# Performance work log

Measured on AMD Instinct MI355X. Metric: run time of the kernel, lower is better.

The kernel has to match this reference:

```python
import jax, jax.numpy as jnp
import numpy as np

N_NODES = 50000
N_EDGES = 600000
IN_F, HID, OUT_F = 602, 128, 41


def _gconv(x, W, b, src, dst, n):
    # DGL GraphConv, norm='both': D_dst^{-1/2} A (D_src^{-1/2} x W) + b
    ones = jnp.ones(src.shape, dtype=x.dtype)
    deg_out = jnp.clip(jax.ops.segment_sum(ones, src, num_segments=n), 1.0)
    deg_in = jnp.clip(jax.ops.segment_sum(ones, dst, num_segments=n), 1.0)
    h = x * jax.lax.rsqrt(deg_out)[:, None]
    h = h @ W  # dense transform first (in_feats > out_feats path)
    agg = jax.ops.segment_sum(h[src], dst, num_segments=n)  # [N, out]
    return agg * jax.lax.rsqrt(deg_in)[:, None] + b


def setup_inputs() -> dict:
    key = jax.random.key(0)
    ks = jax.random.split(key, 8)
    features = jax.random.normal(ks[0], (N_NODES, IN_F), dtype=jnp.float32)
    src = jax.random.randint(ks[1], (N_EDGES,), 0, N_NODES, dtype=jnp.int32)
    dst = jax.random.randint(ks[2], (N_EDGES,), 0, N_NODES, dtype=jnp.int32)
    def glorot(k, fan_in, fan_out):
        s = jnp.sqrt(6.0 / (fan_in + fan_out)).astype(jnp.float32)
        return jax.random.uniform(k, (fan_in, fan_out), jnp.float32, -s, s)
    return {
        'features': features, 'src': src, 'dst': dst,
        'W1': glorot(ks[3], IN_F, HID), 'b1': jnp.zeros((HID,), jnp.float32),
        'W2': glorot(ks[4], HID, HID), 'b2': jnp.zeros((HID,), jnp.float32),
        'W3': glorot(ks[5], HID, HID), 'b3': jnp.zeros((HID,), jnp.float32),
        'Wfc': glorot(ks[6], HID, OUT_F), 'bfc': jnp.zeros((OUT_F,), jnp.float32),
    }


def reference(features, src, dst, W1, b1, W2, b2, W3, b3, Wfc, bfc):
    n = features.shape[0]
    relu = jax.nn.relu
    x = relu(_gconv(features, W1, b1, src, dst, n))  # x = _x
    _x = relu(_gconv(x, W2, b2, src, dst, n))        # branch (layer2)
    x = relu(_gconv(x, W2, b2, src, dst, n))         # main (same layer2)
    x = relu(_gconv(x, W3, b3, src, dst, n))         # layer3
    x = relu(x + _x)                                  # residual + relu
    return x @ Wfc + bfc
```

## Files before the change

### kernel.cpp

```cpp
#include <hip/hip_runtime.h>
#include <hip/hip_bf16.h>

#define NN   50000
#define NE   600000
#define INF  602
#define HID  128
#define OUTF 41
#define NBLK 196

#define GXCD   128
#define GBLKS  (8 * GXCD)
#define GCHUNKS (2 * GXCD)
#define GCHN   ((NN + GCHUNKS - 1) / GCHUNKS)

typedef __attribute__((ext_vector_type(8))) short bf16x8;
typedef __attribute__((ext_vector_type(4))) float f32x4;
typedef __attribute__((ext_vector_type(2))) int i32x2;

__device__ inline unsigned short f2bf(float x) {
    unsigned u = __float_as_uint(x);
    unsigned r = u + 0x7FFF + ((u >> 16) & 1);
    return (unsigned short)(r >> 16);
}

#define GLL16(gp, lp) \
    __builtin_amdgcn_global_load_lds((const __attribute__((address_space(1))) unsigned int*)(gp), \
                                     (__attribute__((address_space(3))) unsigned int*)(lp), 16, 0, 0)

__global__ __launch_bounds__(256) void deg_hist_k(const int* __restrict__ src,
                                                  const int* __restrict__ dst,
                                                  int* __restrict__ cnt_out,
                                                  int* __restrict__ cnt_in, int E) {
    int e = blockIdx.x * 256 + threadIdx.x;
    if (e < E) {
        atomicAdd(&cnt_out[src[e]], 1);
        atomicAdd(&cnt_in[dst[e]], 1);
    }
}

__global__ __launch_bounds__(256) void scan1_k(const int* __restrict__ cnt,
                                               int* __restrict__ rowptr,
                                               int* __restrict__ blockSum) {
    __shared__ int tmp[256];
    int tid = threadIdx.x;
    int i = blockIdx.x * 256 + tid;
    int v = (i < NN) ? cnt[i] : 0;
    tmp[tid] = v;
    __syncthreads();
#pragma unroll
    for (int off = 1; off < 256; off <<= 1) {
        int t = (tid >= off) ? tmp[tid - off] : 0;
        __syncthreads();
        tmp[tid] += t;
        __syncthreads();
    }
    if (i < NN) rowptr[i] = tmp[tid] - v;
    if (tid == 255) blockSum[blockIdx.x] = tmp[255];
}

__global__ __launch_bounds__(256) void scan23_k(int* __restrict__ rowptr,
                                                const int* __restrict__ blockSum,
                                                int* __restrict__ wcur,
                                                const int* __restrict__ cnt_out,
                                                const int* __restrict__ cnt_in,
                                                float* __restrict__ rs_out,
                                                float* __restrict__ rs_in) {
    const int tid = threadIdx.x;
    const int bid = blockIdx.x;
    int vAll = (tid < NBLK) ? blockSum[tid] : 0;
    int vPre = (tid < bid) ? vAll : 0;
#pragma unroll
    for (int o = 32; o; o >>= 1) {
        vAll += __shfl_down(vAll, o);
        vPre += __shfl_down(vPre, o);
    }
    __shared__ int sA[4], sP[4];
    if ((tid & 63) == 0) { sA[tid >> 6] = vAll; sP[tid >> 6] = vPre; }
    __syncthreads();
    int offAll = sA[0] + sA[1] + sA[2] + sA[3];
    int offPre = sP[0] + sP[1] + sP[2] + sP[3];
    int i = bid * 256 + tid;
    if (i < NN) {
        int r = rowptr[i] + offPre;
        rowptr[i] = r;
        wcur[i] = r;
        int co = cnt_out[i]; if (co < 1) co = 1;
        int ci = cnt_in[i];  if (ci < 1) ci = 1;
        rs_out[i] = rsqrtf((float)co);
        rs_in[i]  = rsqrtf((float)ci);
    }
    if (bid == NBLK - 1 && tid == 0) rowptr[NN] = offAll;
}

__global__ __launch_bounds__(256) void fill_csr_k(const int* __restrict__ src,
                                                  const int* __restrict__ dst,
                                                  int* __restrict__ wcur,
                                                  int* __restrict__ csrsrc, int E) {
    int e = blockIdx.x * 256 + threadIdx.x;
    if (e < E) {
        int p = atomicAdd(&wcur[dst[e]], 1);
        csrsrc[p] = src[e];
    }
}

__device__ inline void prep_w_body(const float* __restrict__ W, int K,
                                   unsigned short* __restrict__ out, int total4, int i) {
    if (i >= total4) return;
    int col = i & 127;
    int k4 = (i >> 7) << 2;
    short4 h;
    h.x = (short)f2bf((k4 + 0 < K) ? W[(size_t)(k4 + 0) * HID + col] : 0.f);
    h.y = (short)f2bf((k4 + 1 < K) ? W[(size_t)(k4 + 1) * HID + col] : 0.f);
    h.z = (short)f2bf((k4 + 2 < K) ? W[(size_t)(k4 + 2) * HID + col] : 0.f);
    h.w = (short)f2bf((k4 + 3 < K) ? W[(size_t)(k4 + 3) * HID + col] : 0.f);
    *(short4*)&out[(size_t)(k4 >> 3) * 1024 + col * 8 + (k4 & 7)] = h;
}

__global__ __launch_bounds__(256) void prep_all_k(const float* __restrict__ W1,
                                                  const float* __restrict__ W2,
                                                  const float* __restrict__ W3,
                                                  unsigned short* __restrict__ W1t,
                                                  unsigned short* __restrict__ W2t,
                                                  unsigned short* __restrict__ W3t,
                                                  int* __restrict__ cnt) {
    int b = blockIdx.x;
    if (b < 80) {
        int t = b * 256 + threadIdx.x;
        prep_w_body(W1, INF, W1t, 20480, t);
        for (int i = t; i < 2 * NN; i += 20480) cnt[i] = 0;
    } else if (b < 96) {
        prep_w_body(W2, HID, W2t, 4096, (b - 80) * 256 + threadIdx.x);
    } else {
        prep_w_body(W3, HID, W3t, 4096, (b - 96) * 256 + threadIdx.x);
    }
}

__global__ __launch_bounds__(256) void gemm1_k(const float* __restrict__ A,
                                               const unsigned short* __restrict__ Wt,
                                               const float* __restrict__ rs_out,
                                               unsigned short* __restrict__ H, int n) {
    __shared__ __attribute__((aligned(16))) short As[64 * 136];
    __shared__ __attribute__((aligned(16))) short Bs[16 * 1024];

    const int tid = threadIdx.x;
    const int wave = tid >> 6;
    const int lane = tid & 63;
    const int quad = lane >> 4;
    const int l16 = lane & 15;
    const int rowBase = blockIdx.x * 64;
    const int tileBase = rowBase + wave * 16;

    float4 apf[8];
    auto loadA = [&](int ch) {
        int kb = ch * 128;
#pragma unroll
        for (int c = 0; c < 8; ++c) {
            int f = c * 256 + tid;
            int row = f >> 5;
            int kc = (f & 31) << 2;
            int grow = rowBase + row;
            int gk = kb + kc;
            float4 v = {0.f, 0.f, 0.f, 0.f};
            if (grow < n) {
                if (gk + 3 < INF) {
                    v = *(const float4*)(A + (size_t)grow * INF + gk);
                } else {
                    if (gk + 0 < INF) v.x = A[(size_t)grow * INF + gk + 0];
                    if (gk + 1 < INF) v.y = A[(size_t)grow * INF + gk + 1];
                    if (gk + 2 < INF) v.z = A[(size_t)grow * INF + gk + 2];
                }
            }
            apf[c] = v;
        }
    };
    auto storeA = [&]() {
#pragma unroll
        for (int c = 0; c < 8; ++c) {
            int f = c * 256 + tid;
            int row = f >> 5;
            int kc = (f & 31) << 2;
            short4 h;
            h.x = (short)f2bf(apf[c].x); h.y = (short)f2bf(apf[c].y);
            h.z = (short)f2bf(apf[c].z); h.w = (short)f2bf(apf[c].w);
            *(short4*)&As[row * 136 + kc] = h;
        }
    };
    auto issueB = [&](int ch) {
#pragma unroll
        for (int c = 0; c < 8; ++c)
            GLL16(Wt + (size_t)ch * 16384 + c * 2048 + tid * 8, &Bs[c * 2048 + tid * 8]);
    };

    f32x4 acc[8];
#pragma unroll
    for (int j = 0; j < 8; ++j) acc[j] = (f32x4){0.f, 0.f, 0.f, 0.f};

    loadA(0);
    for (int ch = 0; ch < 5; ++ch) {
        __syncthreads();
        issueB(ch);
        storeA();
        __syncthreads();
        if (ch + 1 < 5) loadA(ch + 1);
#pragma unroll
        for (int s = 0; s < 4; ++s) {
            bf16x8 af = *(const bf16x8*)&As[(wave * 16 + l16) * 136 + s * 32 + quad * 8];
            const short* bg = &Bs[(s * 4 + quad) * 1024 + l16 * 8];
#pragma unroll
            for (int nt = 0; nt < 8; ++nt) {
                bf16x8 bf = *(const bf16x8*)(bg + nt * 128);
                acc[nt] = __builtin_amdgcn_mfma_f32_16x16x32_bf16(af, bf, acc[nt], 0, 0, 0);
            }
        }
    }

#pragma unroll
    for (int r = 0; r < 4; ++r) {
        int row = tileBase + quad * 4 + r;
        if (row < n) {
            float ro = rs_out[row];
#pragma unroll
            for (int nt = 0; nt < 8; ++nt)
                H[(size_t)row * HID + nt * 16 + l16] = f2bf(acc[nt][r] * ro);
        }
    }
}

__global__ __launch_bounds__(256) void gemm_hid_k(const unsigned short* __restrict__ A,
                                                  const unsigned short* __restrict__ Wt,
                                                  unsigned short* __restrict__ H, int n) {
    __shared__ __attribute__((aligned(16))) short As[64 * 136];
    __shared__ __attribute__((aligned(16))) short Bs[16384];

    const int tid = threadIdx.x;
    const int wave = tid >> 6;
    const int lane = tid & 63;
    const int quad = lane >> 4;
    const int l16 = lane & 15;
    const int wm = wave >> 1;
    const int wn = wave & 1;
    const int rowBase = blockIdx.x * 64;

#pragma unroll
    for (int c = 0; c < 8; ++c)
        GLL16(Wt + c * 2048 + tid * 8, &Bs[c * 2048 + tid * 8]);

#pragma unroll
    for (int c = 0; c < 4; ++c) {
        int f = c * 256 + tid;
        int row = f >> 4;
        int k16 = (f & 15) << 3;
        int grow = rowBase + row;
        int4 v = {0, 0, 0, 0};
        if (grow < n) v = *(const int4*)(A + (size_t)grow * HID + k16);
        *(int4*)&As[row * 136 + k16] = v;
    }
    __syncthreads();

    f32x4 acc[2][4];
#pragma unroll
    for (int i = 0; i < 2; ++i)
#pragma unroll
        for (int j = 0; j < 4; ++j) acc[i][j] = (f32x4){0.f, 0.f, 0.f, 0.f};

#pragma unroll
    for (int kq = 0; kq < 4; ++kq) {
        bf16x8 af[2], bfr[4];
#pragma unroll
        for (int mt = 0; mt < 2; ++mt)
            af[mt] = *(const bf16x8*)&As[(wm * 32 + mt * 16 + l16) * 136 + kq * 32 + quad * 8];
#pragma unroll
        for (int nt = 0; nt < 4; ++nt)
            bfr[nt] = *(const bf16x8*)&Bs[(kq * 4 + quad) * 1024 + (wn * 64 + nt * 16 + l16) * 8];
#pragma unroll
        for (int mt = 0; mt < 2; ++mt)
#pragma unroll
            for (int nt = 0; nt < 4; ++nt)
                acc[mt][nt] = __builtin_amdgcn_mfma_f32_16x16x32_bf16(af[mt], bfr[nt], acc[mt][nt], 0, 0, 0);
    }

#pragma unroll
    for (int mt = 0; mt < 2; ++mt)
#pragma unroll
        for (int r = 0; r < 4; ++r) {
            int row = rowBase + wm * 32 + mt * 16 + quad * 4 + r;
            if (row < n) {
#pragma unroll
                for (int nt = 0; nt < 4; ++nt) {
                    int col = wn * 64 + nt * 16 + l16;
                    H[(size_t)row * HID + col] = f2bf(acc[mt][nt][r]);
                }
            }
        }
}

__global__ __launch_bounds__(256) void gath_slice_k(const unsigned short* __restrict__ Hin,
                                                    const int* __restrict__ rowptr,
                                                    const int* __restrict__ csrsrc,
                                                    const float* __restrict__ rs_in,
                                                    const float* __restrict__ rs_out,
                                                    const float* __restrict__ bias,
                                                    const float* __restrict__ residIn,
                                                    float* __restrict__ residOut,
                                                    unsigned short* __restrict__ outXs,
                                                    float* __restrict__ outX,
                                                    int n) {
    const int b = blockIdx.x;
    const int xcd = b & 7;
    const int slice = xcd >> 1;
    const int chunk = ((b >> 3) << 1) + (xcd & 1);
    const int n0 = chunk * GCHN;
    const int n1 = min(n0 + GCHN, n);

    const int tid = threadIdx.x;
    const int wave = tid >> 6;
    const int lane = tid & 63;
    const int g = lane >> 3;
    const int l8 = lane & 7;
    const int gbase = g << 3;
    const int col = slice * 32 + l8 * 4;

    const float4 bb = *(const float4*)(bias + col);

    for (int nb = n0 + wave * 8; nb < n1; nb += 32) {
        int node = nb + g;
        bool alive = node < n1;
        int beg = 0, end = 0;
        if (alive) { beg = rowptr[node]; end = rowptr[node + 1]; }

        float a0 = 0.f, a1 = 0.f, a2 = 0.f, a3 = 0.f;

        for (int base = beg; base < end; base += 8) {
            int m = end - base; if (m > 8) m = 8;
            int idx = (l8 < m) ? csrsrc[base + l8] : 0;
            int j = 0;
            for (; j + 3 < m; j += 4) {
                int s0 = __shfl(idx, gbase | j);
                int s1 = __shfl(idx, gbase | (j + 1));
                int s2 = __shfl(idx, gbase | (j + 2));
                int s3 = __shfl(idx, gbase | (j + 3));
                int2 u0 = *(const int2*)(Hin + (size_t)s0 * HID + col);
                int2 u1 = *(const int2*)(Hin + (size_t)s1 * HID + col);
                int2 u2 = *(const int2*)(Hin + (size_t)s2 * HID + col);
                int2 u3 = *(const int2*)(Hin + (size_t)s3 * HID + col);
#pragma unroll
                for (int q = 0; q < 4; ++q) {
                    int2 u = (q == 0) ? u0 : (q == 1) ? u1 : (q == 2) ? u2 : u3;
                    unsigned x = (unsigned)u.x, y = (unsigned)u.y;
                    a0 += __uint_as_float(x << 16); a1 += __uint_as_float(x & 0xFFFF0000u);
                    a2 += __uint_as_float(y << 16); a3 += __uint_as_float(y & 0xFFFF0000u);
                }
            }
            for (; j < m; ++j) {
                int s = __shfl(idx, gbase | j);
                int2 u = *(const int2*)(Hin + (size_t)s * HID + col);
                unsigned x = (unsigned)u.x, y = (unsigned)u.y;
                a0 += __uint_as_float(x << 16); a1 += __uint_as_float(x & 0xFFFF0000u);
                a2 += __uint_as_float(y << 16); a3 += __uint_as_float(y & 0xFFFF0000u);
            }
        }

        if (alive) {
            float ri = rs_in[node];
            float v0 = fmaxf(a0 * ri + bb.x, 0.f);
            float v1 = fmaxf(a1 * ri + bb.y, 0.f);
            float v2 = fmaxf(a2 * ri + bb.z, 0.f);
            float v3 = fmaxf(a3 * ri + bb.w, 0.f);
            size_t o = (size_t)node * HID + col;
            if (residOut)
                __builtin_nontemporal_store((f32x4){v0, v1, v2, v3}, (f32x4*)(residOut + o));
            if (residIn) {
                f32x4 r = __builtin_nontemporal_load((const f32x4*)(residIn + o));
                v0 = fmaxf(v0 + r[0], 0.f);
                v1 = fmaxf(v1 + r[1], 0.f);
                v2 = fmaxf(v2 + r[2], 0.f);
                v3 = fmaxf(v3 + r[3], 0.f);
            }
            if (outXs) {
                float ro = rs_out[node];
                i32x2 h;
                h[0] = (int)(((unsigned)f2bf(v1 * ro) << 16) | f2bf(v0 * ro));
                h[1] = (int)(((unsigned)f2bf(v3 * ro) << 16) | f2bf(v2 * ro));
                __builtin_nontemporal_store(h, (i32x2*)(outXs + o));
            }
            if (outX)
                __builtin_nontemporal_store((f32x4){v0, v1, v2, v3}, (f32x4*)(outX + o));
        }
    }
}

__global__ __launch_bounds__(256) void fc_k(const float* __restrict__ X,
                                            const float* __restrict__ Wfc,
                                            const float* __restrict__ bfc,
                                            float* __restrict__ out, int n) {
    __shared__ float Ws[HID * OUTF];
    __shared__ float Xs[4][HID];
    int tid = threadIdx.x;
    for (int i = tid; i < HID * OUTF; i += 256) Ws[i] = Wfc[i];
    int rowBase = blockIdx.x * 4;
    for (int i = tid; i < 4 * HID; i += 256) {
        int r = i >> 7, c = i & 127;
        int gr = rowBase + r;
        Xs[r][c] = (gr < n) ? X[(size_t)gr * HID + c] : 0.f;
    }
    __syncthreads();
    int wv = tid >> 6, lane = tid & 63;
    int row = rowBase + wv;
    if (row < n && lane < OUTF) {
        float acc = bfc[lane];
#pragma unroll 8
        for (int k = 0; k < HID; ++k) acc += Xs[wv][k] * Ws[k * OUTF + lane];
        out[(size_t)row * OUTF + lane] = acc;
    }
}

extern "C" void kernel_launch(void* const* d_in, const int* in_sizes, int n_in,
                              void* d_out, int out_size, void* d_ws, size_t ws_size,
                              hipStream_t stream) {
    const float* feat = (const float*)d_in[0];
    const int* src = (const int*)d_in[1];
    const int* dst = (const int*)d_in[2];
    const float* W1 = (const float*)d_in[3];
    const float* b1 = (const float*)d_in[4];
    const float* W2 = (const float*)d_in[5];
    const float* b2 = (const float*)d_in[6];
    const float* W3 = (const float*)d_in[7];
    const float* b3 = (const float*)d_in[8];
    const float* Wfc = (const float*)d_in[9];
    const float* bfc = (const float*)d_in[10];
    float* out = (float*)d_out;

    char* w = (char*)d_ws;
    auto alloc = [&](size_t b) -> void* {
        void* p = (void*)w;
        w += (b + 255) & ~(size_t)255;
        return p;
    };
    int* cnt = (int*)alloc(2 * NN * sizeof(int));
    int* cnt_out = cnt;
    int* cnt_in  = cnt + NN;
    int* rowptr  = (int*)alloc((NN + 1) * sizeof(int));
    int* wcur    = (int*)alloc(NN * sizeof(int));
    int* csrsrc  = (int*)alloc(NE * sizeof(int));
    int* blockSum = (int*)alloc(NBLK * sizeof(int));
    float* rs_out = (float*)alloc(NN * sizeof(float));
    float* rs_in  = (float*)alloc(NN * sizeof(float));
    unsigned short* W1t = (unsigned short*)alloc(10 * 8192 * sizeof(unsigned short));
    unsigned short* W2t = (unsigned short*)alloc(16384 * sizeof(unsigned short));
    unsigned short* W3t = (unsigned short*)alloc(16384 * sizeof(unsigned short));
    unsigned short* Ha = (unsigned short*)alloc((size_t)NN * HID * sizeof(unsigned short));
    unsigned short* Hb = (unsigned short*)alloc((size_t)NN * HID * sizeof(unsigned short));
    unsigned short* Xb = (unsigned short*)alloc((size_t)NN * HID * sizeof(unsigned short));
    float* resid = (float*)alloc((size_t)NN * HID * sizeof(float));
    float* Xfc   = (float*)alloc((size_t)NN * HID * sizeof(float));

    prep_all_k<<<112, 256, 0, stream>>>(W1, W2, W3, W1t, W2t, W3t, cnt);
    deg_hist_k<<<(NE + 255) / 256, 256, 0, stream>>>(src, dst, cnt_out, cnt_in, NE);
    scan1_k<<<NBLK, 256, 0, stream>>>(cnt_in, rowptr, blockSum);
    scan23_k<<<NBLK, 256, 0, stream>>>(rowptr, blockSum, wcur, cnt_out, cnt_in, rs_out, rs_in);
    fill_csr_k<<<(NE + 255) / 256, 256, 0, stream>>>(src, dst, wcur, csrsrc, NE);

    const int gblk = (NN + 63) / 64;
    gemm1_k<<<gblk, 256, 0, stream>>>(feat, W1t, rs_out, Ha, NN);
    gath_slice_k<<<GBLKS, 256, 0, stream>>>(Ha, rowptr, csrsrc, rs_in, rs_out, b1,
                                            nullptr, nullptr, Xb, nullptr, NN);
    gemm_hid_k<<<gblk, 256, 0, stream>>>(Xb, W2t, Hb, NN);
    gath_slice_k<<<GBLKS, 256, 0, stream>>>(Hb, rowptr, csrsrc, rs_in, rs_out, b2,
                                            nullptr, resid, Xb, nullptr, NN);
    gemm_hid_k<<<gblk, 256, 0, stream>>>(Xb, W3t, Ha, NN);
    gath_slice_k<<<GBLKS, 256, 0, stream>>>(Ha, rowptr, csrsrc, rs_in, rs_out, b3,
                                            resid, nullptr, nullptr, Xfc, NN);
    fc_k<<<(NN + 3) / 4, 256, 0, stream>>>(Xfc, Wfc, bfc, out, NN);
}
```

Before: 523.4 us.

## Store GEMM outputs in column-slab layout so each XCD gathers one contiguous slab

The GEMM kernels now write H as four slabs of 32 columns, each laid out as [NN][32], in place of row-major [NN][128]. The gather kernel indexes its XCD's slab directly, so each XCD's working set is one contiguous 3.2 MB region that fits better in its L2. The grid is also doubled (GXCD 256) and CSR index loads are made nontemporal. The cost is scattered 32-byte row segments on the GEMM store side.

```diff
diff --git a/kernel.cpp b/kernel.cpp
--- a/kernel.cpp
+++ b/kernel.cpp
@@ -8,7 +8,9 @@
 #define OUTF 41
 #define NBLK 196
 
-#define GXCD   128
+#define NSLAB  4
+#define SLABF  32
+#define GXCD   256
 #define GBLKS  (8 * GXCD)
 #define GCHUNKS (2 * GXCD)
 #define GCHN   ((NN + GCHUNKS - 1) / GCHUNKS)
@@ -221,7 +223,8 @@
             float ro = rs_out[row];
 #pragma unroll
             for (int nt = 0; nt < 8; ++nt)
-                H[(size_t)row * HID + nt * 16 + l16] = f2bf(acc[nt][r] * ro);
+                H[(size_t)(nt >> 1) * (NN * SLABF) + (size_t)row * SLABF + (nt & 1) * 16 + l16] =
+                    f2bf(acc[nt][r] * ro);
         }
     }
 }
@@ -287,30 +290,32 @@
             if (row < n) {
 #pragma unroll
                 for (int nt = 0; nt < 4; ++nt) {
-                    int col = wn * 64 + nt * 16 + l16;
-                    H[(size_t)row * HID + col] = f2bf(acc[mt][nt][r]);
+                    int cg = wn * 4 + nt;
+                    H[(size_t)(cg >> 1) * (NN * SLABF) + (size_t)row * SLABF + (cg & 1) * 16 + l16] =
+                        f2bf(acc[mt][nt][r]);
                 }
             }
         }
 }
 
-__global__ __launch_bounds__(256) void gath_slice_k(const unsigned short* __restrict__ Hin,
-                                                    const int* __restrict__ rowptr,
-                                                    const int* __restrict__ csrsrc,
-                                                    const float* __restrict__ rs_in,
-                                                    const float* __restrict__ rs_out,
-                                                    const float* __restrict__ bias,
-                                                    const float* __restrict__ residIn,
-                                                    float* __restrict__ residOut,
-                                                    unsigned short* __restrict__ outXs,
-                                                    float* __restrict__ outX,
-                                                    int n) {
+__global__ __launch_bounds__(256) void gath_slab_k(const unsigned short* __restrict__ Hs,
+                                                   const int* __restrict__ rowptr,
+                                                   const int* __restrict__ csrsrc,
+                                                   const float* __restrict__ rs_in,
+                                                   const float* __restrict__ rs_out,
+                                                   const float* __restrict__ bias,
+                                                   const float* __restrict__ residIn,
+                                                   float* __restrict__ residOut,
+                                                   unsigned short* __restrict__ outXs,
+                                                   float* __restrict__ outX,
+                                                   int n) {
     const int b = blockIdx.x;
     const int xcd = b & 7;
     const int slice = xcd >> 1;
     const int chunk = ((b >> 3) << 1) + (xcd & 1);
     const int n0 = chunk * GCHN;
     const int n1 = min(n0 + GCHN, n);
+    const unsigned short* __restrict__ slab = Hs + (size_t)slice * (NN * SLABF);
 
     const int tid = threadIdx.x;
     const int wave = tid >> 6;
@@ -318,7 +323,8 @@
     const int g = lane >> 3;
     const int l8 = lane & 7;
     const int gbase = g << 3;
-    const int col = slice * 32 + l8 * 4;
+    const int colLoc = l8 * 4;
+    const int col = slice * SLABF + colLoc;
 
     const float4 bb = *(const float4*)(bias + col);
 
@@ -332,17 +338,17 @@
 
         for (int base = beg; base < end; base += 8) {
             int m = end - base; if (m > 8) m = 8;
-            int idx = (l8 < m) ? csrsrc[base + l8] : 0;
+            int idx = (l8 < m) ? __builtin_nontemporal_load(csrsrc + base + l8) : 0;
             int j = 0;
             for (; j + 3 < m; j += 4) {
                 int s0 = __shfl(idx, gbase | j);
                 int s1 = __shfl(idx, gbase | (j + 1));
                 int s2 = __shfl(idx, gbase | (j + 2));
                 int s3 = __shfl(idx, gbase | (j + 3));
-                int2 u0 = *(const int2*)(Hin + (size_t)s0 * HID + col);
-                int2 u1 = *(const int2*)(Hin + (size_t)s1 * HID + col);
-                int2 u2 = *(const int2*)(Hin + (size_t)s2 * HID + col);
-                int2 u3 = *(const int2*)(Hin + (size_t)s3 * HID + col);
+                int2 u0 = *(const int2*)(slab + s0 * SLABF + colLoc);
+                int2 u1 = *(const int2*)(slab + s1 * SLABF + colLoc);
+                int2 u2 = *(const int2*)(slab + s2 * SLABF + colLoc);
+                int2 u3 = *(const int2*)(slab + s3 * SLABF + colLoc);
 #pragma unroll
                 for (int q = 0; q < 4; ++q) {
                     int2 u = (q == 0) ? u0 : (q == 1) ? u1 : (q == 2) ? u2 : u3;
@@ -353,7 +359,7 @@
             }
             for (; j < m; ++j) {
                 int s = __shfl(idx, gbase | j);
-                int2 u = *(const int2*)(Hin + (size_t)s * HID + col);
+                int2 u = *(const int2*)(slab + s * SLABF + colLoc);
                 unsigned x = (unsigned)u.x, y = (unsigned)u.y;
                 a0 += __uint_as_float(x << 16); a1 += __uint_as_float(x & 0xFFFF0000u);
                 a2 += __uint_as_float(y << 16); a3 += __uint_as_float(y & 0xFFFF0000u);
@@ -462,13 +468,13 @@
 
     const int gblk = (NN + 63) / 64;
     gemm1_k<<<gblk, 256, 0, stream>>>(feat, W1t, rs_out, Ha, NN);
-    gath_slice_k<<<GBLKS, 256, 0, stream>>>(Ha, rowptr, csrsrc, rs_in, rs_out, b1,
-                                            nullptr, nullptr, Xb, nullptr, NN);
+    gath_slab_k<<<GBLKS, 256, 0, stream>>>(Ha, rowptr, csrsrc, rs_in, rs_out, b1,
+                                           nullptr, nullptr, Xb, nullptr, NN);
     gemm_hid_k<<<gblk, 256, 0, stream>>>(Xb, W2t, Hb, NN);
-    gath_slice_k<<<GBLKS, 256, 0, stream>>>(Hb, rowptr, csrsrc, rs_in, rs_out, b2,
-                                            nullptr, resid, Xb, nullptr, NN);
+    gath_slab_k<<<GBLKS, 256, 0, stream>>>(Hb, rowptr, csrsrc, rs_in, rs_out, b2,
+                                           nullptr, resid, Xb, nullptr, NN);
     gemm_hid_k<<<gblk, 256, 0, stream>>>(Xb, W3t, Ha, NN);
-    gath_slice_k<<<GBLKS, 256, 0, stream>>>(Ha, rowptr, csrsrc, rs_in, rs_out, b3,
-                                            resid, nullptr, nullptr, Xfc, NN);
+    gath_slab_k<<<GBLKS, 256, 0, stream>>>(Ha, rowptr, csrsrc, rs_in, rs_out, b3,
+                                           resid, nullptr, nullptr, Xfc, NN);
     fc_k<<<(NN + 3) / 4, 256, 0, stream>>>(Xfc, Wfc, bfc, out, NN);
 }
```

New measurement: 499.0 us. -4.7%, faster.
